# Performance work log

Measured on AMD Instinct MI355X. Metric: run time of the kernel, lower is better.

## Reference

```python
import jax, jax.numpy as jnp
import numpy as np

H, W = 85, 85
N_HEAD = 8

def layernorm(x, g, b, eps=1e-5):
    m = x.mean(-1, keepdims=True)
    v = ((x - m) ** 2).mean(-1, keepdims=True)
    return (x - m) * jax.lax.rsqrt(v + eps) * g + b


def setup_inputs() -> dict:
    key = jax.random.key(0)
    ks = jax.random.split(key, 12)
    B, C = 8, 256
    N = H * W
    hd = C // N_HEAD
    Ch = C * 4  # mlp_ratio = 4
    init = lambda k, fan_in, sh: (jax.random.normal(k, sh, jnp.float32) / np.float32(np.sqrt(fan_in)))
    d = {}
    d['fx'] = jax.random.normal(ks[0], (B, N, C), jnp.float32)
    # ln_1
    d['ln1_g'] = jnp.ones((C,), jnp.float32); d['ln1_b'] = jnp.zeros((C,), jnp.float32)
    # Galerkin linear attention projections (per-head split of C)
    d['Wq'] = init(ks[1], C, (C, C)); d['bq'] = jnp.zeros((C,), jnp.float32)
    d['Wk'] = init(ks[2], C, (C, C)); d['bk'] = jnp.zeros((C,), jnp.float32)
    d['Wv'] = init(ks[3], C, (C, C)); d['bv'] = jnp.zeros((C,), jnp.float32)
    d['Wo'] = init(ks[4], C, (C, C)); d['bo'] = jnp.zeros((C,), jnp.float32)
    # per-head LayerNorms on K and V (Galerkin normalization replacing softmax)
    d['kln_g'] = jnp.ones((N_HEAD, hd), jnp.float32); d['kln_b'] = jnp.zeros((N_HEAD, hd), jnp.float32)
    d['vln_g'] = jnp.ones((N_HEAD, hd), jnp.float32); d['vln_b'] = jnp.zeros((N_HEAD, hd), jnp.float32)
    # ln_2
    d['ln2_g'] = jnp.ones((C,), jnp.float32); d['ln2_b'] = jnp.zeros((C,), jnp.float32)
    # MLP (n_layers=0, res=False): pre linear + gelu, post linear
    d['W1'] = init(ks[5], C, (C, Ch)); d['b1'] = jnp.zeros((Ch,), jnp.float32)
    d['W2'] = init(ks[6], Ch, (Ch, C)); d['b2'] = jnp.zeros((C,), jnp.float32)
    return d


def reference(fx, ln1_g, ln1_b, Wq, bq, Wk, bk, Wv, bv, Wo, bo,
              kln_g, kln_b, vln_g, vln_b, ln2_g, ln2_b, W1, b1, W2, b2):
    B, N, C = fx.shape
    hd = C // N_HEAD
    x = layernorm(fx, ln1_g, ln1_b)  # [B,N,C]
    # (permute/reshape to image grid and back is a no-op for per-token attention math)
    split = lambda t: t.reshape(B, N, N_HEAD, hd).transpose(0, 2, 1, 3)  # [B,h,N,d]
    q = split(x @ Wq + bq)
    k = split(x @ Wk + bk)
    v = split(x @ Wv + bv)
    # Galerkin: LayerNorm on K and V over head dim, no softmax
    k = layernorm(k, kln_g[None, :, None, :], kln_b[None, :, None, :])
    v = layernorm(v, vln_g[None, :, None, :], vln_b[None, :, None, :])
    kv = jnp.einsum('bhnd,bhne->bhde', k, v) / N  # [B,h,d,d]
    attn = jnp.einsum('bhnd,bhde->bhne', q, kv)   # [B,h,N,d]
    attn = attn.transpose(0, 2, 1, 3).reshape(B, N, C)
    attn = attn @ Wo + bo
    fx = fx + attn  # residual 1
    x2 = layernorm(fx, ln2_g, ln2_b)
    x2 = jax.nn.gelu(x2 @ W1 + b1) @ W2 + b2
    return fx + x2  # residual 2
```

## Files before the change

### kernel.cpp

```cpp
#include <hip/hip_runtime.h>
#include <hip/hip_bf16.h>
#include <stdint.h>

#define B_ 8
#define NTOK 7225
#define MTOT (B_*NTOK)
#define MROWS 58368
#define MT_FULL 226
#define MT_BATCH 29
#define MLP_TILES 904

typedef unsigned short u16;
typedef u16 u16x8 __attribute__((ext_vector_type(8)));
typedef u16 u16x4 __attribute__((ext_vector_type(4)));
typedef __bf16 bf16x8 __attribute__((ext_vector_type(8)));
typedef float f32x4 __attribute__((ext_vector_type(4)));

__device__ inline float bf2f(u16 u){ union{float f;uint32_t i;}c; c.i=((uint32_t)u)<<16; return c.f; }
__device__ inline u16 f2bf(float f){ union{float f;uint32_t i;}c; c.f=f; uint32_t x=c.i;
                                     return (u16)((x + 0x7fffu + ((x>>16)&1u))>>16); }
__device__ inline uint32_t cvt_pk_bf16(float a, float b){
  uint32_t r; asm("v_cvt_pk_bf16_f32 %0, %1, %2" : "=v"(r) : "v"(a), "v"(b)); return r;
}
__device__ inline float gelu_f(float x){
  float t = 0.7978845608028654f * x * (1.0f + 0.044715f*x*x);
  float e = __expf(2.0f*t);
  return x * (1.0f - __builtin_amdgcn_rcpf(e + 1.0f));
}

__device__ inline void gload_lds16(const u16* g, u16* l) {
  __builtin_amdgcn_global_load_lds(
      (__attribute__((address_space(1))) void*)(const_cast<u16*>(g)),
      (__attribute__((address_space(3))) void*)(l), 16, 0, 0);
}

template<int EPI>
__global__ __launch_bounds__(512, 2)
void gemm256(const u16* __restrict__ A, int lda,
             const u16* __restrict__ Bm, int ldb, long bStride,
             const float* __restrict__ bias, int biasStride,
             const float* __restrict__ res,
             void* __restrict__ outp, int ldo,
             int K, int rowsValid, int batchRowStride,
             const float* __restrict__ g2, const float* __restrict__ b2,
             u16* __restrict__ x2out)
{
  __shared__ alignas(16) u16 lds[65536];
  const int tid = threadIdx.x;
  const int wid = tid >> 6, lane = tid & 63;
  const int wm = wid >> 2, wn = wid & 3;

  const int gx = gridDim.x, gy = gridDim.y;
  const int n = gx * gy;
  const int flat = blockIdx.y * gx + blockIdx.x;
  const int qq = n >> 3, rr = n & 7;
  const int xcd = flat & 7, pos = flat >> 3;
  const int swz = (xcd < rr ? xcd*(qq+1) : rr*(qq+1) + (xcd-rr)*qq) + pos;
  const int bx = swz / gy, by = swz % gy;
  const int bz = blockIdx.z;

  const long rowBase = (long)bz * batchRowStride + (long)bx * 256;
  const int colBase = by * 256;
  const u16* Bp = Bm + (long)bz * bStride;
  const float* biasP = bias + bz * biasStride;

  const int srow = lane >> 2;
  const int scol = ((lane & 3) ^ ((lane >> 3) & 3)) * 8;
  const int NT = K >> 6;

  auto stageHalf = [&](int bf, int kt, int sel) {
    const int sub = sel >> 1;
    const int k0 = (kt << 6) + sub*32 + scol;
    u16* base = lds + ((sel & 1) ? 32768 : 0) + (bf*2 + sub)*8192;
#pragma unroll
    for (int i = 0; i < 2; ++i) {
      const int r0 = (wid*2 + i)*16;
      if ((sel & 1) == 0)
        gload_lds16(A + (rowBase + r0 + srow)*(long)lda + k0, base + r0*32);
      else
        gload_lds16(Bp + (long)(colBase + r0 + srow)*ldb + k0, base + r0*32);
    }
  };

  f32x4 acc[8][4] = {};
  bf16x8 afr[4], bfr[4];
  const int lr = lane & 15;
  const int sl = lane >> 4;
  const int sp = (sl ^ ((lr >> 1) & 3)) * 8;

  stageHalf(0, 0, 0); stageHalf(0, 0, 1); stageHalf(0, 0, 2); stageHalf(0, 0, 3);

  for (int kt = 0; kt < NT; ++kt) {
    const int bf = kt & 1;
    const bool st = (kt + 1 < NT);
#pragma unroll
    for (int ph = 0; ph < 4; ++ph) {
      const int sub = ph >> 1, mh = ph & 1;
      if (ph == 0) {
        asm volatile("s_waitcnt vmcnt(4)" ::: "memory");
      } else if (ph == 2) {
        if (kt == NT - 1) asm volatile("s_waitcnt vmcnt(0)" ::: "memory");
        else              asm volatile("s_waitcnt vmcnt(4)" ::: "memory");
      } else {
        asm volatile("s_waitcnt vmcnt(6)" ::: "memory");
      }
      __builtin_amdgcn_s_barrier();
      const u16* Ab = lds + (bf*2 + sub)*8192;
      const u16* Bb = lds + 32768 + (bf*2 + sub)*8192;
      if (mh == 0) {
#pragma unroll
        for (int ni = 0; ni < 4; ++ni)
          bfr[ni] = *reinterpret_cast<const bf16x8*>(&Bb[(wn*64 + ni*16 + lr)*32 + sp]);
      }
#pragma unroll
      for (int i = 0; i < 4; ++i)
        afr[i] = *reinterpret_cast<const bf16x8*>(&Ab[(wm*128 + (mh*4 + i)*16 + lr)*32 + sp]);
      if (st) stageHalf(bf ^ 1, kt + 1, ph);
      asm volatile("s_waitcnt lgkmcnt(0)" ::: "memory");
      __builtin_amdgcn_sched_barrier(0);
      __builtin_amdgcn_s_setprio(1);
#pragma unroll
      for (int i = 0; i < 4; ++i)
#pragma unroll
        for (int ni = 0; ni < 4; ++ni)
          acc[mh*4 + i][ni] =
              __builtin_amdgcn_mfma_f32_16x16x32_bf16(bfr[ni], afr[i], acc[mh*4 + i][ni], 0, 0, 0);
      __builtin_amdgcn_s_setprio(0);
    }
  }

  const int cq = sl * 4;
  if (EPI <= 1) {
    __syncthreads();
#pragma unroll
    for (int mi = 0; mi < 8; ++mi) {
      const int r = wm*128 + mi*16 + lr;
#pragma unroll
      for (int ni = 0; ni < 4; ++ni) {
        const int c = wn*64 + ni*16 + cq;
        f32x4 v = acc[mi][ni] + *reinterpret_cast<const f32x4*>(&biasP[colBase + c]);
        uint2 pk;
        if (EPI == 1) { pk.x = cvt_pk_bf16(gelu_f(v[0]), gelu_f(v[1]));
                        pk.y = cvt_pk_bf16(gelu_f(v[2]), gelu_f(v[3])); }
        else          { pk.x = cvt_pk_bf16(v[0], v[1]); pk.y = cvt_pk_bf16(v[2], v[3]); }
        const int unit = ((c >> 3) ^ (r & 7));
        *reinterpret_cast<uint2*>(lds + r*256 + unit*8 + (c & 7)) = pk;
      }
    }
    __syncthreads();
#pragma unroll
    for (int p = 0; p < 16; ++p) {
      const int idx = p*512 + tid;
      const int r = idx >> 5, u = idx & 31;
      const int phys = u ^ (r & 7);
      u16x8 val = *reinterpret_cast<const u16x8*>(lds + r*256 + phys*8);
      *reinterpret_cast<u16x8*>((u16*)outp + (rowBase + r)*(long)ldo + colBase + u*8) = val;
    }
  } else {
    float* red = reinterpret_cast<float*>(lds);
    __syncthreads();
#pragma unroll
    for (int mi = 0; mi < 8; ++mi) {
      const int r = wm*128 + mi*16 + lr;
      const bool valid = (bx*256 + r < rowsValid);
      const long grow = rowBase + r;
      float s_r = 0.f, q_r = 0.f;
#pragma unroll
      for (int ni = 0; ni < 4; ++ni) {
        const int c0 = wn*64 + ni*16 + cq;
        f32x4 rv = valid ? *reinterpret_cast<const f32x4*>((const float*)res + grow*256 + c0)
                         : f32x4{0.f,0.f,0.f,0.f};
        f32x4 v = acc[mi][ni] + *reinterpret_cast<const f32x4*>(&biasP[c0]) + rv;
        acc[mi][ni] = v;
        s_r += v[0]+v[1]+v[2]+v[3];
        q_r += v[0]*v[0]+v[1]*v[1]+v[2]*v[2]+v[3]*v[3];
      }
      s_r += __shfl_xor(s_r, 16); s_r += __shfl_xor(s_r, 32);
      q_r += __shfl_xor(q_r, 16); q_r += __shfl_xor(q_r, 32);
      if (sl == 0) {
        red[       (wm*4 + wn)*128 + mi*16 + lr] = s_r;
        red[1024 + (wm*4 + wn)*128 + mi*16 + lr] = q_r;
      }
    }
    __syncthreads();
#pragma unroll
    for (int mi = 0; mi < 8; ++mi) {
      const int r = wm*128 + mi*16 + lr;
      if (bx*256 + r >= rowsValid) continue;
      const long grow = rowBase + r;
      const int rb = wm*4*128 + mi*16 + lr;
      float s_t = red[rb] + red[rb+128] + red[rb+256] + red[rb+384];
      float q_t = red[1024+rb] + red[1024+rb+128] + red[1024+rb+256] + red[1024+rb+384];
      const float m = s_t * (1.0f/256.0f);
      const float var = q_t * (1.0f/256.0f) - m*m;
      const float rs = rsqrtf(var + 1e-5f);
#pragma unroll
      for (int ni = 0; ni < 4; ++ni) {
        const int c0 = wn*64 + ni*16 + cq;
        const long oidx = grow*256 + c0;
        f32x4 v = acc[mi][ni];
        *reinterpret_cast<f32x4*>((float*)outp + oidx) = v;
        f32x4 gv = *reinterpret_cast<const f32x4*>(&g2[c0]);
        f32x4 bv = *reinterpret_cast<const f32x4*>(&b2[c0]);
        f32x4 xn = (v - m) * rs * gv + bv;
        uint2 pk; pk.x = cvt_pk_bf16(xn[0], xn[1]); pk.y = cvt_pk_bf16(xn[2], xn[3]);
        *reinterpret_cast<uint2*>(x2out + oidx) = pk;
      }
    }
  }
}

__global__ __launch_bounds__(512, 1)
void mlp_fused3(const u16* __restrict__ x2, const u16* __restrict__ W1t,
                const u16* __restrict__ W2t, const float* __restrict__ b1,
                const float* __restrict__ b2, float* __restrict__ outF,
                int rowsValid)
{
  __shared__ alignas(16) u16 Xs[64*256];
  __shared__ alignas(16) u16 W1b[2][64*256];
  __shared__ alignas(16) u16 W2b[256*64];
  __shared__ alignas(16) u16 Hs[64*64];
  const int tid = threadIdx.x;
  const int wid = tid >> 6, lane = tid & 63;
  const int wm = wid >> 2, wn = wid & 3;
  const int lr = lane & 15, sl = lane >> 4;
  const long rowBase = (long)blockIdx.x * 64;

#pragma unroll
  for (int i = 0; i < 4; ++i) {
    const int u = i*512 + tid;
    const int r = u >> 5, pu = u & 31;
    gload_lds16(x2 + (rowBase + r)*256 + ((pu ^ (r & 31)) << 3), &Xs[u*8]);
  }
  auto stageW1 = [&](int c, int half) {
#pragma unroll
    for (int i = 0; i < 4; ++i) {
      const int u = i*512 + tid;
      const int r = u >> 5, pu = u & 31;
      gload_lds16(W1t + (long)(c*64 + r)*256 + ((pu ^ (r & 31)) << 3), &W1b[half][u*8]);
    }
  };
  auto stageW2 = [&](int c) {
#pragma unroll
    for (int i = 0; i < 4; ++i) {
      const int u = i*512 + tid;
      const int r = u >> 3, pu = u & 7;
      gload_lds16(W2t + (long)r*1024 + c*64 + ((pu ^ (r & 7)) << 3), &W2b[u*8]);
    }
  };
  stageW1(0, 0);

  f32x4 acc2[2][4] = {};
  for (int c = 0; c < 16; ++c) {
    const int half = c & 1;
    const bool st = (c + 1 < 16);
    stageW2(c);
    if (st) stageW1(c + 1, half ^ 1);
    if (st) asm volatile("s_waitcnt vmcnt(8)" ::: "memory");
    else    asm volatile("s_waitcnt vmcnt(4)" ::: "memory");
    __builtin_amdgcn_s_barrier();

    f32x4 acc1[2] = {};
#pragma unroll
    for (int kk = 0; kk < 8; ++kk) {
      const int u = kk*4 + sl;
      const int rB = wn*16 + lr;
      bf16x8 wb = *reinterpret_cast<const bf16x8*>(&W1b[half][(rB*32 + (u ^ (rB & 31)))*8]);
#pragma unroll
      for (int mi = 0; mi < 2; ++mi) {
        const int rA = wm*32 + mi*16 + lr;
        bf16x8 xa = *reinterpret_cast<const bf16x8*>(&Xs[(rA*32 + (u ^ (rA & 31)))*8]);
        acc1[mi] = __builtin_amdgcn_mfma_f32_16x16x32_bf16(wb, xa, acc1[mi], 0, 0, 0);
      }
    }
    const float* b1c = b1 + c*64;
#pragma unroll
    for (int mi = 0; mi < 2; ++mi) {
      const int r = wm*32 + mi*16 + lr;
      const int col = wn*16 + sl*4;
      f32x4 v = acc1[mi] + *reinterpret_cast<const f32x4*>(&b1c[col]);
      uint2 pk; pk.x = cvt_pk_bf16(gelu_f(v[0]), gelu_f(v[1]));
      pk.y = cvt_pk_bf16(gelu_f(v[2]), gelu_f(v[3]));
      const int uw = (col >> 3) ^ (r & 7);
      *reinterpret_cast<uint2*>(&Hs[r*64 + uw*8 + (col & 7)]) = pk;
    }
    if (st) asm volatile("s_waitcnt vmcnt(4) lgkmcnt(0)" ::: "memory");
    else    asm volatile("s_waitcnt vmcnt(0) lgkmcnt(0)" ::: "memory");
    __builtin_amdgcn_s_barrier();

#pragma unroll
    for (int kk2 = 0; kk2 < 2; ++kk2) {
      const int u = kk2*4 + sl;
      bf16x8 ha[2];
#pragma unroll
      for (int mi = 0; mi < 2; ++mi) {
        const int r = wm*32 + mi*16 + lr;
        ha[mi] = *reinterpret_cast<const bf16x8*>(&Hs[(r*8 + (u ^ (r & 7)))*8]);
      }
#pragma unroll
      for (int nj = 0; nj < 4; ++nj) {
        const int rB = wn*64 + nj*16 + lr;
        bf16x8 wb = *reinterpret_cast<const bf16x8*>(&W2b[(rB*8 + (u ^ (rB & 7)))*8]);
#pragma unroll
        for (int mi = 0; mi < 2; ++mi)
          acc2[mi][nj] = __builtin_amdgcn_mfma_f32_16x16x32_bf16(wb, ha[mi], acc2[mi][nj], 0, 0, 0);
      }
    }
    __builtin_amdgcn_s_barrier();
  }
#pragma unroll
  for (int mi = 0; mi < 2; ++mi) {
    const int r = wm*32 + mi*16 + lr;
    if (rowBase + r < rowsValid) {
      float* orow = outF + (rowBase + r)*256;
#pragma unroll
      for (int nj = 0; nj < 4; ++nj) {
        const int col = wn*64 + nj*16 + sl*4;
        f32x4 v = acc2[mi][nj] + *reinterpret_cast<const f32x4*>(&b2[col])
                + *reinterpret_cast<const f32x4*>(&orow[col]);
        *reinterpret_cast<f32x4*>(&orow[col]) = v;
      }
    }
  }
}

__global__ __launch_bounds__(256)
void ln_kernel(const float* __restrict__ in, const float* __restrict__ g,
               const float* __restrict__ bt, u16* __restrict__ out, int M)
{
  const int wv = threadIdx.x >> 6, lane = threadIdx.x & 63;
  const int t = blockIdx.x * 4 + wv;
  if (t >= M) return;
  const float4 x = reinterpret_cast<const float4*>(in + (long)t*256)[lane];
  float s = x.x + x.y + x.z + x.w;
  float q = x.x*x.x + x.y*x.y + x.z*x.z + x.w*x.w;
#pragma unroll
  for (int o = 32; o > 0; o >>= 1) { s += __shfl_xor(s, o); q += __shfl_xor(q, o); }
  const float m  = s * (1.0f/256.0f);
  const float var = q * (1.0f/256.0f) - m*m;
  const float rs = rsqrtf(var + 1e-5f);
  const float4 gv = reinterpret_cast<const float4*>(g)[lane];
  const float4 bv = reinterpret_cast<const float4*>(bt)[lane];
  uint2 o4;
  o4.x = cvt_pk_bf16((x.x - m)*rs*gv.x + bv.x, (x.y - m)*rs*gv.y + bv.y);
  o4.y = cvt_pk_bf16((x.z - m)*rs*gv.z + bv.z, (x.w - m)*rs*gv.w + bv.w);
  *reinterpret_cast<uint2*>(out + (long)t*256 + lane*4) = o4;
}

__global__ __launch_bounds__(256)
void kv_kernel(const u16* __restrict__ KV,
               const float* __restrict__ kg, const float* __restrict__ kb,
               const float* __restrict__ vg, const float* __restrict__ vb,
               float* __restrict__ kvout)
{
  const int bh = blockIdx.x, b = bh >> 3, h = bh & 7;
  const int tid = threadIdx.x;
  __shared__ u16 kls[256][32];
  __shared__ u16 vls[256][32];
  __shared__ float sg[4][32];
  if (tid < 32) {
    sg[0][tid] = kg[h*32 + tid];
    sg[1][tid] = kb[h*32 + tid];
    sg[2][tid] = vg[h*32 + tid];
    sg[3][tid] = vb[h*32 + tid];
  }
  const int d = tid >> 3, e0 = (tid & 7) * 4;
  float a0=0, a1=0, a2=0, a3=0;

  for (int sub = 0; sub < 2; ++sub) {
    const int r = blockIdx.y * 512 + sub * 256 + tid;
    __syncthreads();
    if (r < NTOK) {
      const u16* rowp = KV + (long)(b*NTOK + r)*512;
#pragma unroll
      for (int kv2 = 0; kv2 < 2; ++kv2) {
        const u16* p = rowp + (kv2 ? 256 : 0) + h*32;
        float xv[32]; float s = 0.f;
#pragma unroll
        for (int q4 = 0; q4 < 4; ++q4) {
          u16x8 u = *reinterpret_cast<const u16x8*>(p + q4*8);
#pragma unroll
          for (int j = 0; j < 8; ++j) { float f = bf2f(u[j]); xv[q4*8+j] = f; s += f; }
        }
        const float m = s * (1.0f/32.0f);
        float vv = 0.f;
#pragma unroll
        for (int j = 0; j < 32; ++j) { float d2 = xv[j]-m; vv += d2*d2; }
        const float rs = rsqrtf(vv*(1.0f/32.0f) + 1e-5f);
        const float* gg = sg[kv2 ? 2 : 0];
        const float* bb = sg[kv2 ? 3 : 1];
        u16 (*dst)[32] = kv2 ? vls : kls;
#pragma unroll
        for (int j = 0; j < 32; ++j) dst[tid][j] = f2bf((xv[j]-m)*rs*gg[j] + bb[j]);
      }
    } else {
#pragma unroll
      for (int j = 0; j < 32; ++j) { kls[tid][j] = 0; vls[tid][j] = 0; }
    }
    __syncthreads();
#pragma unroll 4
    for (int rr = 0; rr < 256; ++rr) {
      const float kd = bf2f(kls[rr][d]);
      u16x4 v4 = *reinterpret_cast<const u16x4*>(&vls[rr][e0]);
      a0 += kd * bf2f(v4[0]); a1 += kd * bf2f(v4[1]);
      a2 += kd * bf2f(v4[2]); a3 += kd * bf2f(v4[3]);
    }
  }
  const float sc = 1.0f / (float)NTOK;
  float* o = kvout + (long)bh*1024 + d*32 + e0;
  atomicAdd(o+0, a0*sc); atomicAdd(o+1, a1*sc);
  atomicAdd(o+2, a2*sc); atomicAdd(o+3, a3*sc);
}

__global__ __launch_bounds__(256)
void woeff_kernel(const float* __restrict__ kv, const float* __restrict__ Wo,
                  u16* __restrict__ Woet)
{
  const int b = blockIdx.x >> 8, c = blockIdx.x & 255;
  const int rtid = threadIdx.x;
  const int h = rtid >> 5, dd = rtid & 31;
  const float* kvp = kv + ((long)(b*8 + h)*32 + dd)*32;
  float s = 0.f;
#pragma unroll 8
  for (int e = 0; e < 32; ++e) s += kvp[e] * Wo[(h*32 + e)*256 + c];
  Woet[(long)(b*256 + c)*256 + rtid] = f2bf(s);
}

__global__ __launch_bounds__(256)
void watt_kernel(const u16* __restrict__ wq_bf, const u16* __restrict__ Woet,
                 u16* __restrict__ Watt)
{
  const int b = blockIdx.x >> 8, c = blockIdx.x & 255;
  const int k = threadIdx.x;
  const u16* wr = wq_bf + (long)k*256;
  const u16* er = Woet + ((long)(b*256 + c))*256;
  float s = 0.f;
#pragma unroll 4
  for (int j0 = 0; j0 < 256; j0 += 8) {
    u16x8 wv = *reinterpret_cast<const u16x8*>(wr + j0);
    u16x8 ev = *reinterpret_cast<const u16x8*>(er + j0);
#pragma unroll
    for (int j = 0; j < 8; ++j) s += bf2f(wv[j]) * bf2f(ev[j]);
  }
  Watt[((long)(b*256 + c))*256 + k] = f2bf(s);
}

__global__ __launch_bounds__(256)
void be_kernel(const float* __restrict__ bq, const float* __restrict__ bo,
               const u16* __restrict__ Woet, float* __restrict__ be)
{
  const int b = blockIdx.x, c = threadIdx.x;
  const u16* er = Woet + ((long)(b*256 + c))*256;
  float s = bo[c];
#pragma unroll 4
  for (int j0 = 0; j0 < 256; j0 += 8) {
    u16x8 ev = *reinterpret_cast<const u16x8*>(er + j0);
#pragma unroll
    for (int j = 0; j < 8; ++j) s += bq[j0+j] * bf2f(ev[j]);
  }
  be[b*256 + c] = s;
}

__device__ void transpose_tile(const float* __restrict__ src, u16* __restrict__ dst,
                               int R, int C, int tcx, int trY)
{
  __shared__ float t[32][33];
  const int tc = tcx * 32, tr = trY * 32;
  const int lx = threadIdx.x & 31, ly = threadIdx.x >> 5;
#pragma unroll
  for (int i = 0; i < 32; i += 8)
    t[ly + i][lx] = src[(long)(tr + ly + i)*C + tc + lx];
  __syncthreads();
#pragma unroll
  for (int i = 0; i < 32; i += 8)
    dst[(long)(tc + ly + i)*R + tr + lx] = f2bf(t[lx][ly + i]);
}

__global__ __launch_bounds__(256)
void prep_kernel(const float* __restrict__ Wk, const float* __restrict__ Wv,
                 const float* __restrict__ W1, const float* __restrict__ W2,
                 const float* __restrict__ Wq,
                 const float* __restrict__ bk, const float* __restrict__ bv,
                 u16* __restrict__ Wkv_t, u16* __restrict__ W1_t, u16* __restrict__ W2_t,
                 u16* __restrict__ wq_bf, float* __restrict__ kvb, float* __restrict__ bkv)
{
  int b = blockIdx.x;
  if (b < 256)      { transpose_tile(W1, W1_t, 256, 1024, b & 31, b >> 5); }
  else if (b < 512) { b -= 256; transpose_tile(W2, W2_t, 1024, 256, b & 7, b >> 3); }
  else if (b < 576) { b -= 512; transpose_tile(Wk, Wkv_t,         256, 256, b & 7, b >> 3); }
  else if (b < 640) { b -= 576; transpose_tile(Wv, Wkv_t + 65536, 256, 256, b & 7, b >> 3); }
  else if (b < 648) {
    const int base = (b - 640) * 8192 + threadIdx.x;
#pragma unroll
    for (int i = 0; i < 32; ++i) wq_bf[base + i*256] = f2bf(Wq[base + i*256]);
  } else if (b < 656) {
    const int base = (b - 648) * 8192 + threadIdx.x;
#pragma unroll
    for (int i = 0; i < 32; ++i) kvb[base + i*256] = 0.f;
  } else {
    const int i = threadIdx.x;
    bkv[i] = bk[i]; bkv[256 + i] = bv[i];
  }
}

extern "C" void kernel_launch(void* const* d_in, const int* in_sizes, int n_in,
                              void* d_out, int out_size, void* d_ws, size_t ws_size,
                              hipStream_t stream)
{
  const float* fx    = (const float*)d_in[0];
  const float* ln1_g = (const float*)d_in[1];
  const float* ln1_b = (const float*)d_in[2];
  const float* Wq = (const float*)d_in[3];
  const float* bq = (const float*)d_in[4];
  const float* Wk = (const float*)d_in[5];
  const float* bk = (const float*)d_in[6];
  const float* Wv = (const float*)d_in[7];
  const float* bv = (const float*)d_in[8];
  const float* Wo = (const float*)d_in[9];
  const float* bo = (const float*)d_in[10];
  const float* kg  = (const float*)d_in[11];
  const float* kbb = (const float*)d_in[12];
  const float* vg  = (const float*)d_in[13];
  const float* vbb = (const float*)d_in[14];
  const float* ln2_g = (const float*)d_in[15];
  const float* ln2_b = (const float*)d_in[16];
  const float* W1 = (const float*)d_in[17];
  const float* b1 = (const float*)d_in[18];
  const float* W2 = (const float*)d_in[19];
  const float* b2 = (const float*)d_in[20];
  float* outF = (float*)d_out;

  char* ws = (char*)d_ws;
  size_t off = 0;
  auto alloc = [&](size_t bytes) { char* p = ws + off; off += (bytes + 255) & ~(size_t)255; return p; };
  u16* bufX   = (u16*)alloc((size_t)MROWS*256*2);
  u16* bufKV  = (u16*)alloc((size_t)MROWS*512*2);
  u16* Wkv_t  = (u16*)alloc(512*256*2);
  u16* W1_t   = (u16*)alloc(1024*256*2);
  u16* W2_t   = (u16*)alloc(256*1024*2);
  u16* Woe_t  = (u16*)alloc((size_t)8*256*256*2);
  u16* Watt   = (u16*)alloc((size_t)8*256*256*2);
  u16* wq_bf  = (u16*)alloc(256*256*2);
  float* kvb  = (float*)alloc((size_t)64*1024*4);
  float* bkv  = (float*)alloc(512*4);
  float* be   = (float*)alloc(8*256*4);
  (void)ws_size; (void)out_size; (void)n_in; (void)in_sizes;

  prep_kernel<<<657, 256, 0, stream>>>(Wk, Wv, W1, W2, Wq, bk, bv,
                                       Wkv_t, W1_t, W2_t, wq_bf, kvb, bkv);

  ln_kernel<<<MTOT/4, 256, 0, stream>>>(fx, ln1_g, ln1_b, bufX, MTOT);

  gemm256<0><<<dim3(MT_FULL, 2, 1), 512, 0, stream>>>(
      bufX, 256, Wkv_t, 256, 0, bkv, 0, nullptr, bufKV, 512, 256, MTOT, 0,
      nullptr, nullptr, nullptr);

  kv_kernel<<<dim3(64, 15), 256, 0, stream>>>(bufKV, kg, kbb, vg, vbb, kvb);

  woeff_kernel<<<2048, 256, 0, stream>>>(kvb, Wo, Woe_t);
  watt_kernel<<<2048, 256, 0, stream>>>(wq_bf, Woe_t, Watt);
  be_kernel<<<8, 256, 0, stream>>>(bq, bo, Woe_t, be);

  gemm256<3><<<dim3(MT_BATCH, 1, 8), 512, 0, stream>>>(
      bufX, 256, Watt, 256, 65536, be, 256, fx, outF, 256, 256, NTOK, NTOK,
      ln2_g, ln2_b, bufX);

  mlp_fused3<<<MLP_TILES, 512, 0, stream>>>(bufX, W1_t, W2_t, b1, b2, outF, MTOT);
}
```

Measured before the change: 323.3 us.

## Share one LDS weight buffer in fused MLP to cut shared memory and raise occupancy

```diff
diff --git a/kernel.cpp b/kernel.cpp
--- a/kernel.cpp
+++ b/kernel.cpp
@@ -210,15 +210,14 @@
   }
 }
 
-__global__ __launch_bounds__(512, 1)
-void mlp_fused3(const u16* __restrict__ x2, const u16* __restrict__ W1t,
+__global__ __launch_bounds__(512, 4)
+void mlp_fused4(const u16* __restrict__ x2, const u16* __restrict__ W1t,
                 const u16* __restrict__ W2t, const float* __restrict__ b1,
                 const float* __restrict__ b2, float* __restrict__ outF,
                 int rowsValid)
 {
   __shared__ alignas(16) u16 Xs[64*256];
-  __shared__ alignas(16) u16 W1b[2][64*256];
-  __shared__ alignas(16) u16 W2b[256*64];
+  __shared__ alignas(16) u16 Wb[32768];
   __shared__ alignas(16) u16 Hs[64*64];
   const int tid = threadIdx.x;
   const int wid = tid >> 6, lane = tid & 63;
@@ -232,12 +231,12 @@
     const int r = u >> 5, pu = u & 31;
     gload_lds16(x2 + (rowBase + r)*256 + ((pu ^ (r & 31)) << 3), &Xs[u*8]);
   }
-  auto stageW1 = [&](int c, int half) {
+  auto stageW1 = [&](int c) {
 #pragma unroll
     for (int i = 0; i < 4; ++i) {
       const int u = i*512 + tid;
       const int r = u >> 5, pu = u & 31;
-      gload_lds16(W1t + (long)(c*64 + r)*256 + ((pu ^ (r & 31)) << 3), &W1b[half][u*8]);
+      gload_lds16(W1t + (long)(c*64 + r)*256 + ((pu ^ (r & 31)) << 3), &Wb[u*8]);
     }
   };
   auto stageW2 = [&](int c) {
@@ -245,27 +244,21 @@
     for (int i = 0; i < 4; ++i) {
       const int u = i*512 + tid;
       const int r = u >> 3, pu = u & 7;
-      gload_lds16(W2t + (long)r*1024 + c*64 + ((pu ^ (r & 7)) << 3), &W2b[u*8]);
+      gload_lds16(W2t + (long)r*1024 + c*64 + ((pu ^ (r & 7)) << 3), &Wb[u*8]);
     }
   };
-  stageW1(0, 0);
+  stageW1(0);
+  asm volatile("s_waitcnt vmcnt(0)" ::: "memory");
+  __syncthreads();
 
   f32x4 acc2[2][4] = {};
   for (int c = 0; c < 16; ++c) {
-    const int half = c & 1;
-    const bool st = (c + 1 < 16);
-    stageW2(c);
-    if (st) stageW1(c + 1, half ^ 1);
-    if (st) asm volatile("s_waitcnt vmcnt(8)" ::: "memory");
-    else    asm volatile("s_waitcnt vmcnt(4)" ::: "memory");
-    __builtin_amdgcn_s_barrier();
-
     f32x4 acc1[2] = {};
 #pragma unroll
     for (int kk = 0; kk < 8; ++kk) {
       const int u = kk*4 + sl;
       const int rB = wn*16 + lr;
-      bf16x8 wb = *reinterpret_cast<const bf16x8*>(&W1b[half][(rB*32 + (u ^ (rB & 31)))*8]);
+      bf16x8 wb = *reinterpret_cast<const bf16x8*>(&Wb[(rB*32 + (u ^ (rB & 31)))*8]);
 #pragma unroll
       for (int mi = 0; mi < 2; ++mi) {
         const int rA = wm*32 + mi*16 + lr;
@@ -284,8 +277,10 @@
       const int uw = (col >> 3) ^ (r & 7);
       *reinterpret_cast<uint2*>(&Hs[r*64 + uw*8 + (col & 7)]) = pk;
     }
-    if (st) asm volatile("s_waitcnt vmcnt(4) lgkmcnt(0)" ::: "memory");
-    else    asm volatile("s_waitcnt vmcnt(0) lgkmcnt(0)" ::: "memory");
+    asm volatile("s_waitcnt lgkmcnt(0)" ::: "memory");
+    __builtin_amdgcn_s_barrier();
+    stageW2(c);
+    asm volatile("s_waitcnt vmcnt(0)" ::: "memory");
     __builtin_amdgcn_s_barrier();
 
 #pragma unroll
@@ -300,13 +295,18 @@
 #pragma unroll
       for (int nj = 0; nj < 4; ++nj) {
         const int rB = wn*64 + nj*16 + lr;
-        bf16x8 wb = *reinterpret_cast<const bf16x8*>(&W2b[(rB*8 + (u ^ (rB & 7)))*8]);
+        bf16x8 wb = *reinterpret_cast<const bf16x8*>(&Wb[(rB*8 + (u ^ (rB & 7)))*8]);
 #pragma unroll
         for (int mi = 0; mi < 2; ++mi)
           acc2[mi][nj] = __builtin_amdgcn_mfma_f32_16x16x32_bf16(wb, ha[mi], acc2[mi][nj], 0, 0, 0);
       }
     }
     __builtin_amdgcn_s_barrier();
+    if (c + 1 < 16) {
+      stageW1(c + 1);
+      asm volatile("s_waitcnt vmcnt(0)" ::: "memory");
+      __builtin_amdgcn_s_barrier();
+    }
   }
 #pragma unroll
   for (int mi = 0; mi < 2; ++mi) {
@@ -565,5 +565,5 @@
       bufX, 256, Watt, 256, 65536, be, 256, fx, outF, 256, 256, NTOK, NTOK,
       ln2_g, ln2_b, bufX);
 
-  mlp_fused3<<<MLP_TILES, 512, 0, stream>>>(bufX, W1_t, W2_t, b1, b2, outF, MTOT);
-}
+  mlp_fused4<<<MLP_TILES, 512, 0, stream>>>(bufX, W1_t, W2_t, b1, b2, outF, MTOT);
+}
```

After: 338.8 us. +4.8%, slower.
